# Performance work log

Hardware: AMD Instinct MI355X
Metric: run time of the kernel (lower is better)

## Reference

```python
import jax, jax.numpy as jnp
import numpy as np

# --- static config (matches init_kwargs) ---
B, N, M = 128, 32, 32
C_IMG, NUM_HIDDEN, NUM_CLASSES = 1, 16, 3
INPUT_DIM = C_IMG + NUM_HIDDEN + NUM_CLASSES          # 20
OUT_DIM = NUM_HIDDEN + NUM_CLASSES + 2                # 21 (moving -> 2 action channels)
C_STATE = INPUT_DIM - C_IMG                           # 19
N_NEO, M_NEO = N - 2, M - 2                           # size_neo=None -> N-2
N_ACTIVE, M_ACTIVE = N - 2, M - 2
ITERATIONS = 10
IN_FEAT = 9 * INPUT_DIM + 2                           # 182, position='current'
THRESH = 0.0007


def setup_inputs() -> dict:
    key = jax.random.key(0)
    ks = jax.random.split(key, 7)
    images = jax.random.uniform(ks[0], (B, N, M, C_IMG), dtype=jnp.float32)
    W1 = jax.random.normal(ks[1], (IN_FEAT, 30), dtype=jnp.float32) * 0.08
    b1 = jnp.zeros((30,), jnp.float32)
    W2 = jax.random.normal(ks[2], (30, 30), dtype=jnp.float32) * 0.18
    b2 = jnp.zeros((30,), jnp.float32)
    W3 = jax.random.normal(ks[3], (30, OUT_DIM), dtype=jnp.float32) * 0.18
    b3 = jnp.zeros((OUT_DIM,), jnp.float32)
    return {"images": images, "W1": W1, "b1": b1, "W2": W2, "b2": b2, "W3": W3, "b3": b3}


def _custom_round(a):
    # positive -> +1, negative -> -1 (with deadzone |a| <= 0.0007 -> 0)
    return jnp.where(a > THRESH, 1, jnp.where(a < -THRESH, -1, 0)).astype(jnp.int32)


def _run(images, W1, b1, W2, b2, W3, b3):
    dx = jnp.arange(3)
    b_idx = jnp.arange(B)[:, None, None, None, None]        # (B,1,1,1,1)
    # fixed 3x3 windows into state (comms): state[x:x+3, y:y+3]
    sr = (jnp.arange(N_NEO)[:, None] + dx)[:, None, :, None]  # (Nn,1,3,1)
    sc = (jnp.arange(M_NEO)[:, None] + dx)[None, :, None, :]  # (1,Mn,1,3)
    half_n = N // 2
    half_m = M // 2

    # initial perception matrix: identity grid (N_neo == N_active)
    gx, gy = jnp.meshgrid(jnp.arange(N_NEO), jnp.arange(M_NEO), indexing="ij")
    perc0 = jnp.broadcast_to(jnp.stack([gx, gy], -1).astype(jnp.int32), (B, N_NEO, M_NEO, 2))
    state0 = jnp.zeros((B, N, M, C_STATE), jnp.float32)
    guesses0 = jnp.zeros((B * N_NEO * M_NEO, OUT_DIM), jnp.float32)

    def step(carry, _):
        state, perc, _ = carry
        px = perc[..., 0]  # (B,Nn,Mn) int32
        py = perc[..., 1]
        # dynamic 3x3 image patches at (px, py)
        rows = px[..., None, None] + dx[:, None]            # (B,Nn,Mn,3,1)
        cols = py[..., None, None] + dx[None, :]            # (B,Nn,Mn,1,3)
        perc_patch = images[b_idx, rows, cols, :]           # (B,Nn,Mn,3,3,C_IMG)
        comms = state[:, sr, sc, :]                          # (B,Nn,Mn,3,3,C_STATE)
        feat = jnp.concatenate([perc_patch, comms], axis=-1)  # (B,Nn,Mn,3,3,INPUT_DIM)
        feat = feat.reshape(B * N_NEO * M_NEO, 9 * INPUT_DIM)
        # position='current' features
        pos_x = ((px - half_n) / half_n).astype(jnp.float32).reshape(-1, 1)
        pos_y = ((py - half_m) / half_m).astype(jnp.float32).reshape(-1, 1)
        inp = jnp.concatenate([feat, pos_x, pos_y], axis=-1)  # (B*Nn*Mn, 182)
        h = jax.nn.relu(inp @ W1 + b1)
        h = jax.nn.relu(h @ W2 + b2)
        guesses = h @ W3 + b3                                 # (B*Nn*Mn, 21)
        outputs = guesses.reshape(B, N_NEO, M_NEO, OUT_DIM)
        state = state.at[:, 1:1 + N_NEO, 1:1 + M_NEO, :].add(outputs[..., :C_STATE])
        # movement: round actions to {-1,0,1}, add, clip to [0, N_active-1]
        delta = _custom_round(outputs[..., -2:])
        perc = jnp.clip(perc + delta, 0, N_ACTIVE - 1)
        return (state, perc, guesses), None

    (state, perc, guesses), _ = jax.lax.scan(step, (state0, perc0, guesses0), None, length=ITERATIONS)
    class_state = state[:, 1:1 + N_NEO, 1:1 + M_NEO, -NUM_CLASSES:]
    return class_state, guesses


def reference(images, W1, b1, W2, b2, W3, b3):
    return _run(images, W1, b1, W2, b2, W3, b3)
```

## Files before the change

kernel.cpp:

```cpp
#include <hip/hip_runtime.h>

#define B_      128
#define NPIX    32
#define NNEO    30
#define CPAD    20
#define OUTD    21
#define ITERS   10
#define THRESHV 0.0007f
#define HSTRIDE 31

#define STATE_ELEMS_PAD (B_ * NPIX * NPIX * CPAD)
#define NCELLS      (B_ * NNEO * NNEO)
#define CLASS_ELEMS (NCELLS * 3)

__global__ void nca_init(float* __restrict__ stateA, float* __restrict__ stateB) {
    int idx = blockIdx.x * blockDim.x + threadIdx.x;
    const int total = B_ * 124 * CPAD;
    if (idx >= total) return;
    int c  = idx % CPAD;
    int t2 = idx / CPAD;
    int cellp = t2 % 124;
    int b    = t2 / 124;
    int i, j;
    if (cellp < 32)      { i = 0;  j = cellp; }
    else if (cellp < 64) { i = 31; j = cellp - 32; }
    else { int k = cellp - 64; i = 1 + (k >> 1); j = (k & 1) ? 31 : 0; }
    size_t off = (((size_t)b * NPIX + i) * NPIX + j) * CPAD + c;
    stateA[off] = 0.0f;
    stateB[off] = 0.0f;
}


#define ROW15(A, x, wrp) do { const float xx_ = (x); \
    const float* __restrict__ w_ = (wrp); \
    _Pragma("unroll") for (int o_ = 0; o_ < 15; o_++) (A)[o_] += xx_ * w_[o_]; \
} while (0)

#define ROW12(A, x, wrp) do { const float xx_ = (x); \
    const float* __restrict__ w_ = (wrp); \
    _Pragma("unroll") for (int o_ = 0; o_ < 12; o_++) (A)[o_] += xx_ * w_[o_]; \
} while (0)

#define ROW9(A, x, wrp) do { const float xx_ = (x); \
    const float* __restrict__ w_ = (wrp); \
    _Pragma("unroll") for (int o_ = 0; o_ < 9; o_++) (A)[o_] += xx_ * w_[o_]; \
} while (0)

template<int MODE>
__global__ __launch_bounds__(512, 4)
void nca_step(const float* __restrict__ img,
              const float* __restrict__ W1, const float* __restrict__ b1,
              const float* __restrict__ W2, const float* __restrict__ b2,
              const float* __restrict__ W3, const float* __restrict__ b3,
              const float* __restrict__ state_old, float* __restrict__ state_new,
              int* perc, float* __restrict__ guesses_out,
              float* __restrict__ class_out)
{
    __shared__ float s_state[10 * NPIX * CPAD];
    __shared__ float s_img[NPIX * NPIX];
    __shared__ float s_h[256 * HSTRIDE];

    const int b   = blockIdx.y;
    const int rg  = blockIdx.x;
    const int i0  = rg * 8;
    const int nr  = (rg == 3) ? 6 : 8;
    const int tid = threadIdx.x;
    const int h   = __builtin_amdgcn_readfirstlane(tid >> 8);
    const int cell = tid & 255;
    const int qoff = h * 15;

    if (MODE != 0) {
        const int n4 = (nr + 2) * (NPIX * CPAD / 4);
        const float4* __restrict__ gs4 =
            (const float4*)(state_old + ((size_t)b * NPIX + i0) * (NPIX * CPAD));
        float4* s4 = (float4*)s_state;
        for (int t = tid; t < n4; t += 512) s4[t] = gs4[t];
    }
    if (tid < 256)
        ((float4*)s_img)[tid] = ((const float4*)(img + (size_t)b * NPIX * NPIX))[tid];
    __syncthreads();

    const int cells = nr * NNEO;
    const bool active = cell < cells;

    int r = 0, j = 0, i = 0, gcell = 0, px = 0, py = 0;
    if (active) {
        r = cell / NNEO;
        j = cell - r * NNEO;
        i = i0 + r;
        gcell = (b * NNEO + i) * NNEO + j;
        if (MODE == 0) { px = i; py = j; }
        else           { px = perc[2 * gcell]; py = perc[2 * gcell + 1]; }
    }

    float a1[15];
    {
        float acc[15];
#pragma unroll
        for (int o = 0; o < 15; o++) acc[o] = b1[qoff + o];
        if (active) {
            if (MODE == 0) {
#pragma clang loop unroll(disable)
                for (int pr = 0; pr < 3; pr++) {
#pragma clang loop unroll(disable)
                    for (int pc = 0; pc < 3; pc++) {
                        const float iv = s_img[(px + pr) * NPIX + (py + pc)];
                        ROW15(acc, iv, W1 + (pr * 3 + pc) * 600 + qoff);
                    }
                }
            } else {
#pragma clang loop unroll(disable)
                for (int pr = 0; pr < 3; pr++) {
#pragma clang loop unroll(disable)
                    for (int pc = 0; pc < 3; pc++) {
                        const float iv = s_img[(px + pr) * NPIX + (py + pc)];
                        const float* __restrict__ wp = W1 + (pr * 3 + pc) * 600 + qoff;
                        const float4* __restrict__ sp =
                            (const float4*)&s_state[((r + pr) * NPIX + (j + pc)) * CPAD];
                        const float4 ga = sp[0], gb = sp[1], gc = sp[2],
                                     gd = sp[3], ge = sp[4];
                        ROW15(acc, iv,   wp);
                        ROW15(acc, ga.x, wp + 30);  ROW15(acc, ga.y, wp + 60);
                        ROW15(acc, ga.z, wp + 90);  ROW15(acc, ga.w, wp + 120);
                        ROW15(acc, gb.x, wp + 150); ROW15(acc, gb.y, wp + 180);
                        ROW15(acc, gb.z, wp + 210); ROW15(acc, gb.w, wp + 240);
                        ROW15(acc, gc.x, wp + 270); ROW15(acc, gc.y, wp + 300);
                        ROW15(acc, gc.z, wp + 330); ROW15(acc, gc.w, wp + 360);
                        ROW15(acc, gd.x, wp + 390); ROW15(acc, gd.y, wp + 420);
                        ROW15(acc, gd.z, wp + 450); ROW15(acc, gd.w, wp + 480);
                        ROW15(acc, ge.x, wp + 510); ROW15(acc, ge.y, wp + 540);
                        ROW15(acc, ge.z, wp + 570);
                    }
                }
            }
            const float posx = (float)(px - 16) * 0.0625f;
            const float posy = (float)(py - 16) * 0.0625f;
            ROW15(acc, posx, W1 + 180 * 30 + qoff);
            ROW15(acc, posy, W1 + 181 * 30 + qoff);
        }
#pragma unroll
        for (int o = 0; o < 15; o++) a1[o] = fmaxf(acc[o], 0.0f);
        if (active) {
#pragma unroll
            for (int o = 0; o < 15; o++) s_h[cell * HSTRIDE + qoff + o] = a1[o];
        }
    }
    __syncthreads();

    float h2[15];
    {
        float acc[15];
#pragma unroll
        for (int o = 0; o < 15; o++) acc[o] = b2[qoff + o];
        if (active) {
            if (h == 0) {
#pragma unroll
                for (int k = 0; k < 15; k++)
                    ROW15(acc, a1[k], W2 + k * 30);
#pragma clang loop unroll(disable)
                for (int k = 15; k < 30; k++) {
                    const float x = s_h[cell * HSTRIDE + k];
                    ROW15(acc, x, W2 + k * 30);
                }
            } else {
#pragma clang loop unroll(disable)
                for (int k = 0; k < 15; k++) {
                    const float x = s_h[cell * HSTRIDE + k];
                    ROW15(acc, x, W2 + k * 30 + 15);
                }
#pragma unroll
                for (int k = 0; k < 15; k++)
                    ROW15(acc, a1[k], W2 + (k + 15) * 30 + 15);
            }
        }
#pragma unroll
        for (int o = 0; o < 15; o++) h2[o] = fmaxf(acc[o], 0.0f);
    }
    __syncthreads();
    if (active) {
#pragma unroll
        for (int o = 0; o < 15; o++) s_h[cell * HSTRIDE + qoff + o] = h2[o];
    }
    __syncthreads();

    if (active) {
        const size_t coff = (((size_t)b * NPIX + (i + 1)) * NPIX + (j + 1)) * CPAD;
        const int    lc   = ((r + 1) * NPIX + (j + 1)) * CPAD;
        if (h == 0) {
            float ov[12];
#pragma unroll
            for (int c = 0; c < 12; c++) ov[c] = b3[c];
#pragma unroll
            for (int k = 0; k < 15; k++)
                ROW12(ov, h2[k], W3 + k * 21);
#pragma clang loop unroll(disable)
            for (int k = 15; k < 30; k++) {
                const float x = s_h[cell * HSTRIDE + k];
                ROW12(ov, x, W3 + k * 21);
            }
            if (MODE == 2) {
                float* __restrict__ g = guesses_out + (size_t)gcell * OUTD;
#pragma unroll
                for (int c = 0; c < 12; c++) g[c] = ov[c];
            } else {
                float4* __restrict__ ns4 = (float4*)(state_new + coff);
                if (MODE == 0) {
                    ns4[0] = make_float4(ov[0], ov[1], ov[2],  ov[3]);
                    ns4[1] = make_float4(ov[4], ov[5], ov[6],  ov[7]);
                    ns4[2] = make_float4(ov[8], ov[9], ov[10], ov[11]);
                } else {
                    const float4* __restrict__ cs4 = (const float4*)&s_state[lc];
                    const float4 c0 = cs4[0], c1 = cs4[1], c2 = cs4[2];
                    ns4[0] = make_float4(c0.x + ov[0], c0.y + ov[1],
                                         c0.z + ov[2], c0.w + ov[3]);
                    ns4[1] = make_float4(c1.x + ov[4], c1.y + ov[5],
                                         c1.z + ov[6], c1.w + ov[7]);
                    ns4[2] = make_float4(c2.x + ov[8], c2.y + ov[9],
                                         c2.z + ov[10], c2.w + ov[11]);
                }
            }
        } else {
            float ov[9];
#pragma unroll
            for (int c = 0; c < 9; c++) ov[c] = b3[12 + c];
#pragma clang loop unroll(disable)
            for (int k = 0; k < 15; k++) {
                const float x = s_h[cell * HSTRIDE + k];
                ROW9(ov, x, W3 + k * 21 + 12);
            }
#pragma unroll
            for (int k = 0; k < 15; k++)
                ROW9(ov, h2[k], W3 + (k + 15) * 21 + 12);
            if (MODE == 2) {
                float* __restrict__ g = guesses_out + (size_t)gcell * OUTD;
#pragma unroll
                for (int c = 0; c < 9; c++) g[12 + c] = ov[c];
                const float4 c4 = *(const float4*)&s_state[lc + 16];
                float* __restrict__ cs = class_out + (size_t)gcell * 3;
                cs[0] = c4.x + ov[4];
                cs[1] = c4.y + ov[5];
                cs[2] = c4.z + ov[6];
            } else {
                float4* __restrict__ ns4 = (float4*)(state_new + coff);
                if (MODE == 0) {
                    ns4[3] = make_float4(ov[0], ov[1], ov[2], ov[3]);
                    ns4[4] = make_float4(ov[4], ov[5], ov[6], 0.0f);
                } else {
                    const float4 c3 = *(const float4*)&s_state[lc + 12];
                    const float4 c4 = *(const float4*)&s_state[lc + 16];
                    ns4[3] = make_float4(c3.x + ov[0], c3.y + ov[1],
                                         c3.z + ov[2], c3.w + ov[3]);
                    ns4[4] = make_float4(c4.x + ov[4], c4.y + ov[5],
                                         c4.z + ov[6], 0.0f);
                }
                int dxm = (ov[7] > THRESHV) ? 1 : ((ov[7] < -THRESHV) ? -1 : 0);
                int dym = (ov[8] > THRESHV) ? 1 : ((ov[8] < -THRESHV) ? -1 : 0);
                px += dxm; py += dym;
                px = (px < 0) ? 0 : ((px > NNEO - 1) ? NNEO - 1 : px);
                py = (py < 0) ? 0 : ((py > NNEO - 1) ? NNEO - 1 : py);
                perc[2 * gcell + 0] = px;
                perc[2 * gcell + 1] = py;
            }
        }
    }
}

extern "C" void kernel_launch(void* const* d_in, const int* in_sizes, int n_in,
                              void* d_out, int out_size, void* d_ws, size_t ws_size,
                              hipStream_t stream) {
    const float* img = (const float*)d_in[0];
    const float* W1  = (const float*)d_in[1];
    const float* b1  = (const float*)d_in[2];
    const float* W2  = (const float*)d_in[3];
    const float* b2  = (const float*)d_in[4];
    const float* W3  = (const float*)d_in[5];
    const float* b3  = (const float*)d_in[6];

    float* out = (float*)d_out;
    float* class_out   = out;
    float* guesses_out = out + CLASS_ELEMS;

    float* stateA = (float*)d_ws;
    float* stateB = stateA + STATE_ELEMS_PAD;
    int*   perc   = (int*)(stateB + STATE_ELEMS_PAD);

    {
        const int total = B_ * 124 * CPAD;
        nca_init<<<(total + 255) / 256, 256, 0, stream>>>(stateA, stateB);
    }

    const dim3 grid(4, B_);
    nca_step<0><<<grid, 512, 0, stream>>>(img, W1, b1, W2, b2, W3, b3,
                                          stateA, stateB, perc,
                                          guesses_out, class_out);
    for (int t = 1; t < ITERS - 1; t++) {
        const float* so = (t & 1) ? stateB : stateA;
        float*       sn = (t & 1) ? stateA : stateB;
        nca_step<1><<<grid, 512, 0, stream>>>(img, W1, b1, W2, b2, W3, b3,
                                              so, sn, perc,
                                              guesses_out, class_out);
    }
    nca_step<2><<<grid, 512, 0, stream>>>(img, W1, b1, W2, b2, W3, b3,
                                          stateB, stateA, perc,
                                          guesses_out, class_out);
}
```

Measured before the change: 336.4 us.

## Switch state to channel-planar layout and flatten cell grid, dropping shared-memory staging

Changes the state buffer from pixel-interleaved 20-channel padding to channel-planar 19×1024 planes, and maps 128 cells per 256-thread block over a flat cell index instead of 8-row groups per image. The shared-memory staging of state and image is removed, so neighbourhood values are read directly from global memory with coalesced per-channel loads and software double-buffered patch loads. This also removes the idle threads that the old partial last row group left. In exchange, the 9x overlapping reads of each patch now go through cache rather than LDS, and each step issues many more scalar global loads.

```diff
diff --git a/kernel.cpp b/kernel.cpp
--- a/kernel.cpp
+++ b/kernel.cpp
@@ -3,33 +3,34 @@
 #define B_      128
 #define NPIX    32
 #define NNEO    30
-#define CPAD    20
+#define NCH     19
+#define PLANE   1024
 #define OUTD    21
 #define ITERS   10
 #define THRESHV 0.0007f
 #define HSTRIDE 31
 
-#define STATE_ELEMS_PAD (B_ * NPIX * NPIX * CPAD)
+#define STATE_ELEMS (B_ * NCH * PLANE)
 #define NCELLS      (B_ * NNEO * NNEO)
 #define CLASS_ELEMS (NCELLS * 3)
 
+
 __global__ void nca_init(float* __restrict__ stateA, float* __restrict__ stateB) {
     int idx = blockIdx.x * blockDim.x + threadIdx.x;
-    const int total = B_ * 124 * CPAD;
+    const int total = B_ * 124 * NCH;
     if (idx >= total) return;
-    int c  = idx % CPAD;
-    int t2 = idx / CPAD;
+    int c  = idx % NCH;
+    int t2 = idx / NCH;
     int cellp = t2 % 124;
     int b    = t2 / 124;
     int i, j;
     if (cellp < 32)      { i = 0;  j = cellp; }
     else if (cellp < 64) { i = 31; j = cellp - 32; }
     else { int k = cellp - 64; i = 1 + (k >> 1); j = (k & 1) ? 31 : 0; }
-    size_t off = (((size_t)b * NPIX + i) * NPIX + j) * CPAD + c;
+    size_t off = ((size_t)(b * NCH + c)) * PLANE + i * NPIX + j;
     stateA[off] = 0.0f;
     stateB[off] = 0.0f;
 }
-
 
 #define ROW15(A, x, wrp) do { const float xx_ = (x); \
     const float* __restrict__ w_ = (wrp); \
@@ -46,8 +47,30 @@
     _Pragma("unroll") for (int o_ = 0; o_ < 9; o_++) (A)[o_] += xx_ * w_[o_]; \
 } while (0)
 
+struct P20 { float c[NCH]; float iv; };
+
+__device__ __forceinline__ P20 loadp(const float* __restrict__ sb,
+                                     const float* __restrict__ ib,
+                                     int i, int j, int px, int py,
+                                     int pr, int pc) {
+    P20 p;
+    const int poff = (i + pr) * NPIX + (j + pc);
+#pragma unroll
+    for (int ch = 0; ch < NCH; ch++) p.c[ch] = sb[ch * PLANE + poff];
+    p.iv = ib[(px + pr) * NPIX + (py + pc)];
+    return p;
+}
+
+__device__ __forceinline__ void fmap15(float* acc, const P20& p,
+                                       const float* __restrict__ wp) {
+    ROW15(acc, p.iv, wp);
+#pragma unroll
+    for (int ch = 0; ch < NCH; ch++)
+        ROW15(acc, p.c[ch], wp + (ch + 1) * 30);
+}
+
 template<int MODE>
-__global__ __launch_bounds__(512, 4)
+__global__ __launch_bounds__(256, 4)
 void nca_step(const float* __restrict__ img,
               const float* __restrict__ W1, const float* __restrict__ b1,
               const float* __restrict__ W2, const float* __restrict__ b2,
@@ -56,94 +79,69 @@
               int* perc, float* __restrict__ guesses_out,
               float* __restrict__ class_out)
 {
-    __shared__ float s_state[10 * NPIX * CPAD];
-    __shared__ float s_img[NPIX * NPIX];
-    __shared__ float s_h[256 * HSTRIDE];
-
-    const int b   = blockIdx.y;
-    const int rg  = blockIdx.x;
-    const int i0  = rg * 8;
-    const int nr  = (rg == 3) ? 6 : 8;
-    const int tid = threadIdx.x;
-    const int h   = __builtin_amdgcn_readfirstlane(tid >> 8);
-    const int cell = tid & 255;
+    __shared__ float s_h[2][128 * HSTRIDE];
+
+    const int tid  = threadIdx.x;
+    const int h    = __builtin_amdgcn_readfirstlane(tid >> 7);
+    const int cl   = tid & 127;
+    const int cell = blockIdx.x * 128 + cl;
     const int qoff = h * 15;
 
-    if (MODE != 0) {
-        const int n4 = (nr + 2) * (NPIX * CPAD / 4);
-        const float4* __restrict__ gs4 =
-            (const float4*)(state_old + ((size_t)b * NPIX + i0) * (NPIX * CPAD));
-        float4* s4 = (float4*)s_state;
-        for (int t = tid; t < n4; t += 512) s4[t] = gs4[t];
-    }
-    if (tid < 256)
-        ((float4*)s_img)[tid] = ((const float4*)(img + (size_t)b * NPIX * NPIX))[tid];
-    __syncthreads();
-
-    const int cells = nr * NNEO;
-    const bool active = cell < cells;
-
-    int r = 0, j = 0, i = 0, gcell = 0, px = 0, py = 0;
-    if (active) {
-        r = cell / NNEO;
-        j = cell - r * NNEO;
-        i = i0 + r;
-        gcell = (b * NNEO + i) * NNEO + j;
-        if (MODE == 0) { px = i; py = j; }
-        else           { px = perc[2 * gcell]; py = perc[2 * gcell + 1]; }
-    }
+    const int b  = cell / (NNEO * NNEO);
+    const int ij = cell - b * (NNEO * NNEO);
+    const int i  = ij / NNEO;
+    const int j  = ij - i * NNEO;
+
+    int px, py;
+    if (MODE == 0) { px = i; py = j; }
+    else           { px = perc[2 * cell]; py = perc[2 * cell + 1]; }
+
+    const float* __restrict__ sb = state_old + (size_t)b * (NCH * PLANE);
+    const float* __restrict__ ib = img + (size_t)b * PLANE;
 
     float a1[15];
     {
         float acc[15];
 #pragma unroll
         for (int o = 0; o < 15; o++) acc[o] = b1[qoff + o];
-        if (active) {
-            if (MODE == 0) {
-#pragma clang loop unroll(disable)
-                for (int pr = 0; pr < 3; pr++) {
-#pragma clang loop unroll(disable)
-                    for (int pc = 0; pc < 3; pc++) {
-                        const float iv = s_img[(px + pr) * NPIX + (py + pc)];
-                        ROW15(acc, iv, W1 + (pr * 3 + pc) * 600 + qoff);
-                    }
+
+        if (MODE == 0) {
+#pragma clang loop unroll(disable)
+            for (int pr = 0; pr < 3; pr++) {
+#pragma clang loop unroll(disable)
+                for (int pc = 0; pc < 3; pc++) {
+                    const float iv = ib[(px + pr) * NPIX + (py + pc)];
+                    ROW15(acc, iv, W1 + (pr * 3 + pc) * 600 + qoff);
                 }
-            } else {
-#pragma clang loop unroll(disable)
-                for (int pr = 0; pr < 3; pr++) {
-#pragma clang loop unroll(disable)
-                    for (int pc = 0; pc < 3; pc++) {
-                        const float iv = s_img[(px + pr) * NPIX + (py + pc)];
-                        const float* __restrict__ wp = W1 + (pr * 3 + pc) * 600 + qoff;
-                        const float4* __restrict__ sp =
-                            (const float4*)&s_state[((r + pr) * NPIX + (j + pc)) * CPAD];
-                        const float4 ga = sp[0], gb = sp[1], gc = sp[2],
-                                     gd = sp[3], ge = sp[4];
-                        ROW15(acc, iv,   wp);
-                        ROW15(acc, ga.x, wp + 30);  ROW15(acc, ga.y, wp + 60);
-                        ROW15(acc, ga.z, wp + 90);  ROW15(acc, ga.w, wp + 120);
-                        ROW15(acc, gb.x, wp + 150); ROW15(acc, gb.y, wp + 180);
-                        ROW15(acc, gb.z, wp + 210); ROW15(acc, gb.w, wp + 240);
-                        ROW15(acc, gc.x, wp + 270); ROW15(acc, gc.y, wp + 300);
-                        ROW15(acc, gc.z, wp + 330); ROW15(acc, gc.w, wp + 360);
-                        ROW15(acc, gd.x, wp + 390); ROW15(acc, gd.y, wp + 420);
-                        ROW15(acc, gd.z, wp + 450); ROW15(acc, gd.w, wp + 480);
-                        ROW15(acc, ge.x, wp + 510); ROW15(acc, ge.y, wp + 540);
-                        ROW15(acc, ge.z, wp + 570);
-                    }
-                }
-            }
-            const float posx = (float)(px - 16) * 0.0625f;
-            const float posy = (float)(py - 16) * 0.0625f;
-            ROW15(acc, posx, W1 + 180 * 30 + qoff);
-            ROW15(acc, posy, W1 + 181 * 30 + qoff);
-        }
+            }
+        } else {
+            P20 pa = loadp(sb, ib, i, j, px, py, 0, 0);
+            P20 pb = loadp(sb, ib, i, j, px, py, 0, 1);
+            fmap15(acc, pa, W1 + 0 * 600 + qoff);
+            pa = loadp(sb, ib, i, j, px, py, 0, 2);
+            fmap15(acc, pb, W1 + 1 * 600 + qoff);
+            pb = loadp(sb, ib, i, j, px, py, 1, 0);
+            fmap15(acc, pa, W1 + 2 * 600 + qoff);
+            pa = loadp(sb, ib, i, j, px, py, 1, 1);
+            fmap15(acc, pb, W1 + 3 * 600 + qoff);
+            pb = loadp(sb, ib, i, j, px, py, 1, 2);
+            fmap15(acc, pa, W1 + 4 * 600 + qoff);
+            pa = loadp(sb, ib, i, j, px, py, 2, 0);
+            fmap15(acc, pb, W1 + 5 * 600 + qoff);
+            pb = loadp(sb, ib, i, j, px, py, 2, 1);
+            fmap15(acc, pa, W1 + 6 * 600 + qoff);
+            pa = loadp(sb, ib, i, j, px, py, 2, 2);
+            fmap15(acc, pb, W1 + 7 * 600 + qoff);
+            fmap15(acc, pa, W1 + 8 * 600 + qoff);
+        }
+        const float posx = (float)(px - 16) * 0.0625f;
+        const float posy = (float)(py - 16) * 0.0625f;
+        ROW15(acc, posx, W1 + 180 * 30 + qoff);
+        ROW15(acc, posy, W1 + 181 * 30 + qoff);
 #pragma unroll
         for (int o = 0; o < 15; o++) a1[o] = fmaxf(acc[o], 0.0f);
-        if (active) {
-#pragma unroll
-            for (int o = 0; o < 15; o++) s_h[cell * HSTRIDE + qoff + o] = a1[o];
-        }
+#pragma unroll
+        for (int o = 0; o < 15; o++) s_h[0][cl * HSTRIDE + qoff + o] = a1[o];
     }
     __syncthreads();
 
@@ -152,115 +150,98 @@
         float acc[15];
 #pragma unroll
         for (int o = 0; o < 15; o++) acc[o] = b2[qoff + o];
-        if (active) {
-            if (h == 0) {
-#pragma unroll
-                for (int k = 0; k < 15; k++)
-                    ROW15(acc, a1[k], W2 + k * 30);
-#pragma clang loop unroll(disable)
-                for (int k = 15; k < 30; k++) {
-                    const float x = s_h[cell * HSTRIDE + k];
-                    ROW15(acc, x, W2 + k * 30);
-                }
+        if (h == 0) {
+#pragma unroll
+            for (int k = 0; k < 15; k++)
+                ROW15(acc, a1[k], W2 + k * 30);
+#pragma clang loop unroll(disable)
+            for (int k = 15; k < 30; k++) {
+                const float x = s_h[0][cl * HSTRIDE + k];
+                ROW15(acc, x, W2 + k * 30);
+            }
+        } else {
+#pragma clang loop unroll(disable)
+            for (int k = 0; k < 15; k++) {
+                const float x = s_h[0][cl * HSTRIDE + k];
+                ROW15(acc, x, W2 + k * 30 + 15);
+            }
+#pragma unroll
+            for (int k = 0; k < 15; k++)
+                ROW15(acc, a1[k], W2 + (k + 15) * 30 + 15);
+        }
+#pragma unroll
+        for (int o = 0; o < 15; o++) h2[o] = fmaxf(acc[o], 0.0f);
+#pragma unroll
+        for (int o = 0; o < 15; o++) s_h[1][cl * HSTRIDE + qoff + o] = h2[o];
+    }
+    __syncthreads();
+
+    const int cen = (i + 1) * NPIX + (j + 1);
+    if (h == 0) {
+        float ov[12];
+#pragma unroll
+        for (int c = 0; c < 12; c++) ov[c] = b3[c];
+#pragma unroll
+        for (int k = 0; k < 15; k++)
+            ROW12(ov, h2[k], W3 + k * 21);
+#pragma clang loop unroll(disable)
+        for (int k = 15; k < 30; k++) {
+            const float x = s_h[1][cl * HSTRIDE + k];
+            ROW12(ov, x, W3 + k * 21);
+        }
+        if (MODE == 2) {
+            float* __restrict__ g = guesses_out + (size_t)cell * OUTD;
+#pragma unroll
+            for (int c = 0; c < 12; c++) g[c] = ov[c];
+        } else {
+            float* __restrict__ sn = state_new + (size_t)b * (NCH * PLANE) + cen;
+            const float* __restrict__ so = sb + cen;
+            if (MODE == 0) {
+#pragma unroll
+                for (int c = 0; c < 12; c++) sn[c * PLANE] = ov[c];
             } else {
-#pragma clang loop unroll(disable)
-                for (int k = 0; k < 15; k++) {
-                    const float x = s_h[cell * HSTRIDE + k];
-                    ROW15(acc, x, W2 + k * 30 + 15);
-                }
-#pragma unroll
-                for (int k = 0; k < 15; k++)
-                    ROW15(acc, a1[k], W2 + (k + 15) * 30 + 15);
-            }
-        }
-#pragma unroll
-        for (int o = 0; o < 15; o++) h2[o] = fmaxf(acc[o], 0.0f);
-    }
-    __syncthreads();
-    if (active) {
-#pragma unroll
-        for (int o = 0; o < 15; o++) s_h[cell * HSTRIDE + qoff + o] = h2[o];
-    }
-    __syncthreads();
-
-    if (active) {
-        const size_t coff = (((size_t)b * NPIX + (i + 1)) * NPIX + (j + 1)) * CPAD;
-        const int    lc   = ((r + 1) * NPIX + (j + 1)) * CPAD;
-        if (h == 0) {
-            float ov[12];
-#pragma unroll
-            for (int c = 0; c < 12; c++) ov[c] = b3[c];
-#pragma unroll
-            for (int k = 0; k < 15; k++)
-                ROW12(ov, h2[k], W3 + k * 21);
-#pragma clang loop unroll(disable)
-            for (int k = 15; k < 30; k++) {
-                const float x = s_h[cell * HSTRIDE + k];
-                ROW12(ov, x, W3 + k * 21);
-            }
-            if (MODE == 2) {
-                float* __restrict__ g = guesses_out + (size_t)gcell * OUTD;
-#pragma unroll
-                for (int c = 0; c < 12; c++) g[c] = ov[c];
+#pragma unroll
+                for (int c = 0; c < 12; c++) sn[c * PLANE] = so[c * PLANE] + ov[c];
+            }
+        }
+    } else {
+        float ov[9];
+#pragma unroll
+        for (int c = 0; c < 9; c++) ov[c] = b3[12 + c];
+#pragma clang loop unroll(disable)
+        for (int k = 0; k < 15; k++) {
+            const float x = s_h[1][cl * HSTRIDE + k];
+            ROW9(ov, x, W3 + k * 21 + 12);
+        }
+#pragma unroll
+        for (int k = 0; k < 15; k++)
+            ROW9(ov, h2[k], W3 + (k + 15) * 21 + 12);
+        if (MODE == 2) {
+            float* __restrict__ g = guesses_out + (size_t)cell * OUTD;
+#pragma unroll
+            for (int c = 0; c < 9; c++) g[12 + c] = ov[c];
+            float* __restrict__ cs = class_out + (size_t)cell * 3;
+#pragma unroll
+            for (int cc = 0; cc < 3; cc++)
+                cs[cc] = sb[(16 + cc) * PLANE + cen] + ov[4 + cc];
+        } else {
+            float* __restrict__ sn = state_new + (size_t)b * (NCH * PLANE) + cen;
+            const float* __restrict__ so = sb + cen;
+            if (MODE == 0) {
+#pragma unroll
+                for (int c = 0; c < 7; c++) sn[(12 + c) * PLANE] = ov[c];
             } else {
-                float4* __restrict__ ns4 = (float4*)(state_new + coff);
-                if (MODE == 0) {
-                    ns4[0] = make_float4(ov[0], ov[1], ov[2],  ov[3]);
-                    ns4[1] = make_float4(ov[4], ov[5], ov[6],  ov[7]);
-                    ns4[2] = make_float4(ov[8], ov[9], ov[10], ov[11]);
-                } else {
-                    const float4* __restrict__ cs4 = (const float4*)&s_state[lc];
-                    const float4 c0 = cs4[0], c1 = cs4[1], c2 = cs4[2];
-                    ns4[0] = make_float4(c0.x + ov[0], c0.y + ov[1],
-                                         c0.z + ov[2], c0.w + ov[3]);
-                    ns4[1] = make_float4(c1.x + ov[4], c1.y + ov[5],
-                                         c1.z + ov[6], c1.w + ov[7]);
-                    ns4[2] = make_float4(c2.x + ov[8], c2.y + ov[9],
-                                         c2.z + ov[10], c2.w + ov[11]);
-                }
-            }
-        } else {
-            float ov[9];
-#pragma unroll
-            for (int c = 0; c < 9; c++) ov[c] = b3[12 + c];
-#pragma clang loop unroll(disable)
-            for (int k = 0; k < 15; k++) {
-                const float x = s_h[cell * HSTRIDE + k];
-                ROW9(ov, x, W3 + k * 21 + 12);
-            }
-#pragma unroll
-            for (int k = 0; k < 15; k++)
-                ROW9(ov, h2[k], W3 + (k + 15) * 21 + 12);
-            if (MODE == 2) {
-                float* __restrict__ g = guesses_out + (size_t)gcell * OUTD;
-#pragma unroll
-                for (int c = 0; c < 9; c++) g[12 + c] = ov[c];
-                const float4 c4 = *(const float4*)&s_state[lc + 16];
-                float* __restrict__ cs = class_out + (size_t)gcell * 3;
-                cs[0] = c4.x + ov[4];
-                cs[1] = c4.y + ov[5];
-                cs[2] = c4.z + ov[6];
-            } else {
-                float4* __restrict__ ns4 = (float4*)(state_new + coff);
-                if (MODE == 0) {
-                    ns4[3] = make_float4(ov[0], ov[1], ov[2], ov[3]);
-                    ns4[4] = make_float4(ov[4], ov[5], ov[6], 0.0f);
-                } else {
-                    const float4 c3 = *(const float4*)&s_state[lc + 12];
-                    const float4 c4 = *(const float4*)&s_state[lc + 16];
-                    ns4[3] = make_float4(c3.x + ov[0], c3.y + ov[1],
-                                         c3.z + ov[2], c3.w + ov[3]);
-                    ns4[4] = make_float4(c4.x + ov[4], c4.y + ov[5],
-                                         c4.z + ov[6], 0.0f);
-                }
-                int dxm = (ov[7] > THRESHV) ? 1 : ((ov[7] < -THRESHV) ? -1 : 0);
-                int dym = (ov[8] > THRESHV) ? 1 : ((ov[8] < -THRESHV) ? -1 : 0);
-                px += dxm; py += dym;
-                px = (px < 0) ? 0 : ((px > NNEO - 1) ? NNEO - 1 : px);
-                py = (py < 0) ? 0 : ((py > NNEO - 1) ? NNEO - 1 : py);
-                perc[2 * gcell + 0] = px;
-                perc[2 * gcell + 1] = py;
-            }
+#pragma unroll
+                for (int c = 0; c < 7; c++)
+                    sn[(12 + c) * PLANE] = so[(12 + c) * PLANE] + ov[c];
+            }
+            int dxm = (ov[7] > THRESHV) ? 1 : ((ov[7] < -THRESHV) ? -1 : 0);
+            int dym = (ov[8] > THRESHV) ? 1 : ((ov[8] < -THRESHV) ? -1 : 0);
+            px += dxm; py += dym;
+            px = (px < 0) ? 0 : ((px > NNEO - 1) ? NNEO - 1 : px);
+            py = (py < 0) ? 0 : ((py > NNEO - 1) ? NNEO - 1 : py);
+            perc[2 * cell + 0] = px;
+            perc[2 * cell + 1] = py;
         }
     }
 }
@@ -281,26 +262,26 @@
     float* guesses_out = out + CLASS_ELEMS;
 
     float* stateA = (float*)d_ws;
-    float* stateB = stateA + STATE_ELEMS_PAD;
-    int*   perc   = (int*)(stateB + STATE_ELEMS_PAD);
+    float* stateB = stateA + STATE_ELEMS;
+    int*   perc   = (int*)(stateB + STATE_ELEMS);
 
     {
-        const int total = B_ * 124 * CPAD;
+        const int total = B_ * 124 * NCH;
         nca_init<<<(total + 255) / 256, 256, 0, stream>>>(stateA, stateB);
     }
 
-    const dim3 grid(4, B_);
-    nca_step<0><<<grid, 512, 0, stream>>>(img, W1, b1, W2, b2, W3, b3,
+    const int grid = NCELLS / 128;
+    nca_step<0><<<grid, 256, 0, stream>>>(img, W1, b1, W2, b2, W3, b3,
                                           stateA, stateB, perc,
                                           guesses_out, class_out);
     for (int t = 1; t < ITERS - 1; t++) {
         const float* so = (t & 1) ? stateB : stateA;
         float*       sn = (t & 1) ? stateA : stateB;
-        nca_step<1><<<grid, 512, 0, stream>>>(img, W1, b1, W2, b2, W3, b3,
+        nca_step<1><<<grid, 256, 0, stream>>>(img, W1, b1, W2, b2, W3, b3,
                                               so, sn, perc,
                                               guesses_out, class_out);
     }
-    nca_step<2><<<grid, 512, 0, stream>>>(img, W1, b1, W2, b2, W3, b3,
+    nca_step<2><<<grid, 256, 0, stream>>>(img, W1, b1, W2, b2, W3, b3,
                                           stateB, stateA, perc,
                                           guesses_out, class_out);
 }
```

Measured after the change: 478.6 us. +42.3%, slower.

## Switch state storage from channel-last padded to channel-planar layout

Applied to the files above, without the earlier changes.

Stores the 19-channel state as planar channel-major (per-batch planes of 32x32) in global and shared memory instead of interleaved cells padded to 20 channels. Shared-memory reads in the first layer become scalar strided loads per channel that map consecutive lanes to consecutive addresses, which avoids the LDS bank conflicts of the 80-byte-stride float4 reads. Global writes become coalesced per channel across cells, and the padding channel is no longer stored. The trade-off is 19 scalar LDS loads per patch position instead of 5 float4 loads, and per-channel scalar global stores.

```diff
diff --git a/kernel.cpp b/kernel.cpp
--- a/kernel.cpp
+++ b/kernel.cpp
@@ -3,33 +3,36 @@
 #define B_      128
 #define NPIX    32
 #define NNEO    30
-#define CPAD    20
+#define NCH     19
+#define PLANE   1024
+#define SROWS   10
+#define SPLANE  (SROWS * NPIX)
 #define OUTD    21
 #define ITERS   10
 #define THRESHV 0.0007f
 #define HSTRIDE 31
 
-#define STATE_ELEMS_PAD (B_ * NPIX * NPIX * CPAD)
+#define STATE_ELEMS (B_ * NCH * PLANE)
 #define NCELLS      (B_ * NNEO * NNEO)
 #define CLASS_ELEMS (NCELLS * 3)
 
+
 __global__ void nca_init(float* __restrict__ stateA, float* __restrict__ stateB) {
     int idx = blockIdx.x * blockDim.x + threadIdx.x;
-    const int total = B_ * 124 * CPAD;
+    const int total = B_ * 124 * NCH;
     if (idx >= total) return;
-    int c  = idx % CPAD;
-    int t2 = idx / CPAD;
+    int c  = idx % NCH;
+    int t2 = idx / NCH;
     int cellp = t2 % 124;
     int b    = t2 / 124;
     int i, j;
     if (cellp < 32)      { i = 0;  j = cellp; }
     else if (cellp < 64) { i = 31; j = cellp - 32; }
     else { int k = cellp - 64; i = 1 + (k >> 1); j = (k & 1) ? 31 : 0; }
-    size_t off = (((size_t)b * NPIX + i) * NPIX + j) * CPAD + c;
+    size_t off = ((size_t)(b * NCH + c)) * PLANE + i * NPIX + j;
     stateA[off] = 0.0f;
     stateB[off] = 0.0f;
 }
-
 
 #define ROW15(A, x, wrp) do { const float xx_ = (x); \
     const float* __restrict__ w_ = (wrp); \
@@ -56,7 +59,7 @@
               int* perc, float* __restrict__ guesses_out,
               float* __restrict__ class_out)
 {
-    __shared__ float s_state[10 * NPIX * CPAD];
+    __shared__ float s_state[NCH * SPLANE];
     __shared__ float s_img[NPIX * NPIX];
     __shared__ float s_h[256 * HSTRIDE];
 
@@ -70,14 +73,23 @@
     const int qoff = h * 15;
 
     if (MODE != 0) {
-        const int n4 = (nr + 2) * (NPIX * CPAD / 4);
-        const float4* __restrict__ gs4 =
-            (const float4*)(state_old + ((size_t)b * NPIX + i0) * (NPIX * CPAD));
+        const float4* __restrict__ g4 = (const float4*)
+            (state_old + (size_t)b * (NCH * PLANE) + i0 * NPIX);
         float4* s4 = (float4*)s_state;
-        for (int t = tid; t < n4; t += 512) s4[t] = gs4[t];
+        if (nr == 8) {
+            for (int t = tid; t < NCH * 80; t += 512) {
+                const int ch = t / 80, rem = t - ch * 80;
+                s4[ch * 80 + rem] = g4[ch * 256 + rem];
+            }
+        } else {
+            for (int t = tid; t < NCH * 64; t += 512) {
+                const int ch = t / 64, rem = t - ch * 64;
+                s4[ch * 80 + rem] = g4[ch * 256 + rem];
+            }
+        }
     }
     if (tid < 256)
-        ((float4*)s_img)[tid] = ((const float4*)(img + (size_t)b * NPIX * NPIX))[tid];
+        ((float4*)s_img)[tid] = ((const float4*)(img + (size_t)b * PLANE))[tid];
     __syncthreads();
 
     const int cells = nr * NNEO;
@@ -114,22 +126,17 @@
 #pragma clang loop unroll(disable)
                     for (int pc = 0; pc < 3; pc++) {
                         const float iv = s_img[(px + pr) * NPIX + (py + pc)];
-                        const float* __restrict__ wp = W1 + (pr * 3 + pc) * 600 + qoff;
-                        const float4* __restrict__ sp =
-                            (const float4*)&s_state[((r + pr) * NPIX + (j + pc)) * CPAD];
-                        const float4 ga = sp[0], gb = sp[1], gc = sp[2],
-                                     gd = sp[3], ge = sp[4];
-                        ROW15(acc, iv,   wp);
-                        ROW15(acc, ga.x, wp + 30);  ROW15(acc, ga.y, wp + 60);
-                        ROW15(acc, ga.z, wp + 90);  ROW15(acc, ga.w, wp + 120);
-                        ROW15(acc, gb.x, wp + 150); ROW15(acc, gb.y, wp + 180);
-                        ROW15(acc, gb.z, wp + 210); ROW15(acc, gb.w, wp + 240);
-                        ROW15(acc, gc.x, wp + 270); ROW15(acc, gc.y, wp + 300);
-                        ROW15(acc, gc.z, wp + 330); ROW15(acc, gc.w, wp + 360);
-                        ROW15(acc, gd.x, wp + 390); ROW15(acc, gd.y, wp + 420);
-                        ROW15(acc, gd.z, wp + 450); ROW15(acc, gd.w, wp + 480);
-                        ROW15(acc, ge.x, wp + 510); ROW15(acc, ge.y, wp + 540);
-                        ROW15(acc, ge.z, wp + 570);
+                        const float* __restrict__ wp =
+                            W1 + (pr * 3 + pc) * 600 + qoff;
+                        const int soff = (r + pr) * NPIX + (j + pc);
+                        float fv[NCH];
+#pragma unroll
+                        for (int ch = 0; ch < NCH; ch++)
+                            fv[ch] = s_state[ch * SPLANE + soff];
+                        ROW15(acc, iv, wp);
+#pragma unroll
+                        for (int ch = 0; ch < NCH; ch++)
+                            ROW15(acc, fv[ch], wp + (ch + 1) * 30);
                     }
                 }
             }
@@ -184,8 +191,10 @@
     __syncthreads();
 
     if (active) {
-        const size_t coff = (((size_t)b * NPIX + (i + 1)) * NPIX + (j + 1)) * CPAD;
-        const int    lc   = ((r + 1) * NPIX + (j + 1)) * CPAD;
+        const int cen  = (i + 1) * NPIX + (j + 1);
+        const int lcen = (r + 1) * NPIX + (j + 1);
+        float* __restrict__ snp =
+            state_new + (size_t)b * (NCH * PLANE) + cen;
         if (h == 0) {
             float ov[12];
 #pragma unroll
@@ -202,22 +211,13 @@
                 float* __restrict__ g = guesses_out + (size_t)gcell * OUTD;
 #pragma unroll
                 for (int c = 0; c < 12; c++) g[c] = ov[c];
+            } else if (MODE == 0) {
+#pragma unroll
+                for (int c = 0; c < 12; c++) snp[c * PLANE] = ov[c];
             } else {
-                float4* __restrict__ ns4 = (float4*)(state_new + coff);
-                if (MODE == 0) {
-                    ns4[0] = make_float4(ov[0], ov[1], ov[2],  ov[3]);
-                    ns4[1] = make_float4(ov[4], ov[5], ov[6],  ov[7]);
-                    ns4[2] = make_float4(ov[8], ov[9], ov[10], ov[11]);
-                } else {
-                    const float4* __restrict__ cs4 = (const float4*)&s_state[lc];
-                    const float4 c0 = cs4[0], c1 = cs4[1], c2 = cs4[2];
-                    ns4[0] = make_float4(c0.x + ov[0], c0.y + ov[1],
-                                         c0.z + ov[2], c0.w + ov[3]);
-                    ns4[1] = make_float4(c1.x + ov[4], c1.y + ov[5],
-                                         c1.z + ov[6], c1.w + ov[7]);
-                    ns4[2] = make_float4(c2.x + ov[8], c2.y + ov[9],
-                                         c2.z + ov[10], c2.w + ov[11]);
-                }
+#pragma unroll
+                for (int c = 0; c < 12; c++)
+                    snp[c * PLANE] = s_state[c * SPLANE + lcen] + ov[c];
             }
         } else {
             float ov[9];
@@ -235,23 +235,19 @@
                 float* __restrict__ g = guesses_out + (size_t)gcell * OUTD;
 #pragma unroll
                 for (int c = 0; c < 9; c++) g[12 + c] = ov[c];
-                const float4 c4 = *(const float4*)&s_state[lc + 16];
                 float* __restrict__ cs = class_out + (size_t)gcell * 3;
-                cs[0] = c4.x + ov[4];
-                cs[1] = c4.y + ov[5];
-                cs[2] = c4.z + ov[6];
+#pragma unroll
+                for (int cc = 0; cc < 3; cc++)
+                    cs[cc] = s_state[(16 + cc) * SPLANE + lcen] + ov[4 + cc];
             } else {
-                float4* __restrict__ ns4 = (float4*)(state_new + coff);
                 if (MODE == 0) {
-                    ns4[3] = make_float4(ov[0], ov[1], ov[2], ov[3]);
-                    ns4[4] = make_float4(ov[4], ov[5], ov[6], 0.0f);
+#pragma unroll
+                    for (int c = 0; c < 7; c++) snp[(12 + c) * PLANE] = ov[c];
                 } else {
-                    const float4 c3 = *(const float4*)&s_state[lc + 12];
-                    const float4 c4 = *(const float4*)&s_state[lc + 16];
-                    ns4[3] = make_float4(c3.x + ov[0], c3.y + ov[1],
-                                         c3.z + ov[2], c3.w + ov[3]);
-                    ns4[4] = make_float4(c4.x + ov[4], c4.y + ov[5],
-                                         c4.z + ov[6], 0.0f);
+#pragma unroll
+                    for (int c = 0; c < 7; c++)
+                        snp[(12 + c) * PLANE] =
+                            s_state[(12 + c) * SPLANE + lcen] + ov[c];
                 }
                 int dxm = (ov[7] > THRESHV) ? 1 : ((ov[7] < -THRESHV) ? -1 : 0);
                 int dym = (ov[8] > THRESHV) ? 1 : ((ov[8] < -THRESHV) ? -1 : 0);
@@ -281,11 +277,11 @@
     float* guesses_out = out + CLASS_ELEMS;
 
     float* stateA = (float*)d_ws;
-    float* stateB = stateA + STATE_ELEMS_PAD;
-    int*   perc   = (int*)(stateB + STATE_ELEMS_PAD);
+    float* stateB = stateA + STATE_ELEMS;
+    int*   perc   = (int*)(stateB + STATE_ELEMS);
 
     {
-        const int total = B_ * 124 * CPAD;
+        const int total = B_ * 124 * NCH;
         nca_init<<<(total + 255) / 256, 256, 0, stream>>>(stateA, stateB);
     }
 
```

After: 382.5 us. 13.7% more time.
